# Kernel tuning notes

Measured on AMD Instinct MI355X. Metric: run time of the kernel, lower is better.

## Reference

```python
import jax, jax.numpy as jnp
import numpy as np

N = 100000   # total nodes in batch
E = 1200000  # total edges
D = 64       # dim_features (== hidden_dim)
H = 64       # hidden_dim
T = 32       # dim_targets
L = 3        # num_layers
G = 500      # number of graphs in batch


def setup_inputs() -> dict:
    key = jax.random.key(0)
    ks = jax.random.split(key, 16)
    s = 0.1
    inp = {
        "x": jax.random.normal(ks[0], (N, D), jnp.float32),
        "src": jax.random.randint(ks[1], (E,), 0, N, jnp.int32),
        "dst": jax.random.randint(ks[2], (E,), 0, N, jnp.int32),
        "graph_ids": jnp.sort(jax.random.randint(ks[3], (N,), 0, G, jnp.int32)),
        # GINConv learnable eps (init 0)
        "eps": jnp.zeros((L,), jnp.float32),
        # per-layer conv apply MLP: Linear(D->H), ReLU, Linear(H->H)
        "conv_w1": jax.random.normal(ks[4], (L, D, H), jnp.float32) * s,
        "conv_b1": jnp.zeros((L, H), jnp.float32),
        "conv_w2": jax.random.normal(ks[5], (L, H, H), jnp.float32) * s,
        "conv_b2": jnp.zeros((L, H), jnp.float32),
        # GraphNorm params
        "gn_weight": jnp.ones((L, H), jnp.float32),
        "gn_bias": jnp.zeros((L, H), jnp.float32),
        "gn_scale": jnp.ones((L, H), jnp.float32),
        # per-layer projection MLP: Linear(H->H), ReLU, Linear(H->T)
        "proj_w1": jax.random.normal(ks[6], (L, H, H), jnp.float32) * s,
        "proj_b1": jnp.zeros((L, H), jnp.float32),
        "proj_w2": jax.random.normal(ks[7], (L, H, T), jnp.float32) * s,
        "proj_b2": jnp.zeros((L, T), jnp.float32),
    }
    return inp


def reference(x, src, dst, graph_ids, eps, conv_w1, conv_b1, conv_w2, conv_b2,
              gn_weight, gn_bias, gn_scale, proj_w1, proj_b1, proj_w2, proj_b2):
    gid = graph_ids
    counts = jax.ops.segment_sum(jnp.ones((N,), x.dtype), gid, num_segments=G)
    safe = jnp.maximum(counts, 1.0)[:, None]  # [G,1] nodes per graph

    feat = x
    outs = []
    for l in range(L):
        # GINConv: (1+eps)*h_i + sum over incoming neighbors
        agg = jax.ops.segment_sum(feat[src], dst, num_segments=N)
        h = (1.0 + eps[l]) * feat + agg
        h = jnp.maximum(h @ conv_w1[l] + conv_b1[l], 0.0) @ conv_w2[l] + conv_b2[l]
        # GraphNorm: per-graph mean/std
        mean = jax.ops.segment_sum(h, gid, num_segments=G) / safe
        sub = h - mean[gid] * gn_scale[l]
        var = jax.ops.segment_sum(sub * sub, gid, num_segments=G) / safe
        std = jnp.sqrt(var + 1e-8)
        h = gn_weight[l] * sub / std[gid] + gn_bias[l]
        feat = jnp.maximum(h, 0.0)
        # projection MLP + per-graph mean pooling
        z = jnp.maximum(feat @ proj_w1[l] + proj_b1[l], 0.0) @ proj_w2[l] + proj_b2[l]
        outs.append(jax.ops.segment_sum(z, gid, num_segments=G) / safe)
    return jnp.concatenate(outs, axis=-1)  # [G, L*T]
```

## Files before the change

### kernel.cpp

```cpp
#include <hip/hip_runtime.h>
#include <math.h>

#define N_NODES 100000
#define N_EDGES 1200000
#define DIM 64
#define TDIM 32
#define NLAYERS 3
#define NGRAPH 500
#define NP (N_NODES + 1)

#define BUCKW 512
#define NBUCK ((N_NODES + BUCKW - 1) / BUCKW)
#define ECHUNK ((N_EDGES + 255) / 256)
#define MLPBL ((N_NODES + 63) / 64)

typedef unsigned short bfu;
typedef __attribute__((ext_vector_type(8))) short short8;
typedef __attribute__((ext_vector_type(4))) float v4f;

__device__ __forceinline__ float bf2f(bfu u) {
    union { unsigned int i; float f; } v; v.i = ((unsigned int)u) << 16; return v.f;
}
__device__ __forceinline__ float bflo(unsigned int d) {
    union { unsigned int i; float f; } v; v.i = d << 16; return v.f;
}
__device__ __forceinline__ float bfhi(unsigned int d) {
    union { unsigned int i; float f; } v; v.i = d & 0xFFFF0000u; return v.f;
}
__device__ __forceinline__ bfu f2bf(float f) {
    union { float f; unsigned int i; } v; v.f = f;
    unsigned int r = v.i + 0x7FFFu + ((v.i >> 16) & 1u);
    return (bfu)(r >> 16);
}

__global__ __launch_bounds__(256) void k_setup(const float* __restrict__ x, bfu* __restrict__ xb,
                                               const int* __restrict__ gid, int* __restrict__ gstart,
                                               float* __restrict__ inv_safe, float* __restrict__ ncnt,
                                               const float* __restrict__ w1, const float* __restrict__ w2,
                                               const float* __restrict__ q1, const float* __restrict__ q2,
                                               bfu* __restrict__ w1t, bfu* __restrict__ w2t,
                                               bfu* __restrict__ q1t, bfu* __restrict__ q2t,
                                               const int* __restrict__ dst, int* __restrict__ bcnt) {
    int b = blockIdx.x, t = threadIdx.x;
    if (b < 6250) {
        int base = (b * 256 + t) * 4;
        float4 v = *(const float4*)&x[base];
        ushort4 o;
        o.x = f2bf(v.x); o.y = f2bf(v.y); o.z = f2bf(v.z); o.w = f2bf(v.w);
        *(ushort4*)&xb[base] = o;
    } else if (b == 6250) {
        for (int tt = t; tt <= NGRAPH; tt += 256) {
            int lo = 0, hi = N_NODES;
            while (lo < hi) {
                int mid = (lo + hi) >> 1;
                if (gid[mid] < tt) lo = mid + 1; else hi = mid;
            }
            gstart[tt] = lo;
        }
        __syncthreads();
        for (int tt = t; tt < NGRAPH; tt += 256) {
            int c = gstart[tt + 1] - gstart[tt];
            inv_safe[tt] = 1.0f / (float)(c > 1 ? c : 1);
            ncnt[tt] = (float)c;
        }
    } else if (b < 6299) {
        int i = (b - 6251) * 256 + t;
        int l = i >> 12, k = (i >> 6) & 63, n = i & 63;
        int o = (l << 12) | (n << 6) | k;
        w1t[o] = f2bf(w1[i]);
        w2t[o] = f2bf(w2[i]);
        q1t[o] = f2bf(q1[i]);
        if (i < NLAYERS * 2048) {
            int l2 = i >> 11, rem = i & 2047, k2 = rem >> 5, n2 = rem & 31;
            q2t[l2 * 2048 + n2 * 64 + k2] = f2bf(q2[i]);
        }
    } else {
        __shared__ int h[NBUCK];
        for (int i = t; i < NBUCK; i += 256) h[i] = 0;
        __syncthreads();
        int e0 = (b - 6299) * ECHUNK;
        int e1 = e0 + ECHUNK; if (e1 > N_EDGES) e1 = N_EDGES;
        for (int e = e0 + t; e < e1; e += 256) atomicAdd(&h[dst[e] >> 9], 1);
        __syncthreads();
        for (int i = t; i < NBUCK; i += 256) if (h[i]) atomicAdd(&bcnt[i], h[i]);
    }
}

__global__ __launch_bounds__(256) void k_bscan(const int* __restrict__ bcnt,
                                               int* __restrict__ bbase, int* __restrict__ bcursor,
                                               const int* __restrict__ gstart,
                                               const float* __restrict__ pb2all, float* __restrict__ out) {
    __shared__ int s[256];
    int t = threadIdx.x;
    s[t] = (t < NBUCK) ? bcnt[t] : 0;
    __syncthreads();
    for (int off = 1; off < 256; off <<= 1) {
        int v = (t >= off) ? s[t - off] : 0;
        __syncthreads();
        s[t] += v;
        __syncthreads();
    }
    int ex = t ? s[t - 1] : 0;
    if (t < NBUCK) { bbase[t] = ex; bcursor[t] = ex; }
    if (t == 0) bbase[NBUCK] = N_EDGES;
    for (int g = t; g < NGRAPH; g += 256) {
        int nn = gstart[g + 1] - gstart[g];
        for (int r = 0; r < NLAYERS * TDIM; r++)
            out[g * (NLAYERS * TDIM) + r] = (nn > 0) ? pb2all[r] : 0.f;
    }
}

__global__ __launch_bounds__(256) void k_bscatter(const int* __restrict__ src, const int* __restrict__ dst,
                                                  int* __restrict__ bcursor, int2* __restrict__ ebuf) {
    __shared__ int cnt[NBUCK];
    __shared__ int base[NBUCK];
    int t = threadIdx.x;
    for (int i = t; i < NBUCK; i += 256) cnt[i] = 0;
    __syncthreads();
    int e0 = blockIdx.x * ECHUNK;
    int e1 = e0 + ECHUNK; if (e1 > N_EDGES) e1 = N_EDGES;
    for (int e = e0 + t; e < e1; e += 256) atomicAdd(&cnt[dst[e] >> 9], 1);
    __syncthreads();
    for (int i = t; i < NBUCK; i += 256) base[i] = cnt[i] ? atomicAdd(&bcursor[i], cnt[i]) : 0;
    __syncthreads();
    for (int i = t; i < NBUCK; i += 256) cnt[i] = 0;
    __syncthreads();
    for (int e = e0 + t; e < e1; e += 256) {
        int d = dst[e];
        int b = d >> 9;
        int r = atomicAdd(&cnt[b], 1);
        ebuf[base[b] + r] = make_int2(src[e], d);
    }
}

__global__ __launch_bounds__(256) void k_bcsr(const int2* __restrict__ ebuf, const int* __restrict__ bbase,
                                              int* __restrict__ offs, int* __restrict__ csr) {
    __shared__ int ldeg[BUCKW];
    __shared__ int lscan[BUCKW];
    __shared__ int lcur[BUCKW];
    int t = threadIdx.x;
    int b = blockIdx.x;
    int nbase = b << 9;
    int ebeg = bbase[b], eend = bbase[b + 1];
    ldeg[t] = 0; ldeg[t + 256] = 0;
    __syncthreads();
    for (int e = ebeg + t; e < eend; e += 256) atomicAdd(&ldeg[ebuf[e].y - nbase], 1);
    __syncthreads();
    lscan[t] = ldeg[t]; lscan[t + 256] = ldeg[t + 256];
    __syncthreads();
    for (int off = 1; off < BUCKW; off <<= 1) {
        int i0 = t, i1 = t + 256;
        int v0 = (i0 >= off) ? lscan[i0 - off] : 0;
        int v1 = (i1 >= off) ? lscan[i1 - off] : 0;
        __syncthreads();
        lscan[i0] += v0; lscan[i1] += v1;
        __syncthreads();
    }
    int ex0 = lscan[t] - ldeg[t];
    int ex1 = lscan[t + 256] - ldeg[t + 256];
    lcur[t] = ex0; lcur[t + 256] = ex1;
    int n0 = nbase + t, n1 = nbase + t + 256;
    if (n0 < N_NODES) offs[n0] = ebeg + ex0;
    if (n1 < N_NODES) offs[n1] = ebeg + ex1;
    if (b == 0 && t == 0) offs[N_NODES] = N_EDGES;
    __syncthreads();
    for (int e = ebeg + t; e < eend; e += 256) {
        int2 p = ebuf[e];
        int slot = atomicAdd(&lcur[p.y - nbase], 1);
        csr[ebeg + slot] = p.x;
    }
}

__global__ __launch_bounds__(256) void k_agg(const bfu* __restrict__ feat, const int* __restrict__ offs,
                                             const int* __restrict__ csr, const float* __restrict__ eps,
                                             int l, bfu* __restrict__ hin) {
    int t = threadIdx.x;
    int sub = t & 15;
    int node = blockIdx.x * 16 + (t >> 4);
    if (node >= N_NODES) return;
    int coff = sub * 4;
    int e0 = offs[node], e1 = offs[node + 1];
    int eL = e1 - 1;
    float acc0 = 0.f, acc1 = 0.f, acc2 = 0.f, acc3 = 0.f;

    for (int e = e0; e < e1; e += 2) {
        int eb = e + 1;
        int cb = (eb < e1) ? eb : eL;
        int sa = csr[e];
        int sb = csr[cb];
        uint2 da = *(const uint2*)&feat[sa * DIM + coff];
        uint2 db = *(const uint2*)&feat[sb * DIM + coff];
        if (eb >= e1) { db.x = 0u; db.y = 0u; }
        acc0 += bflo(da.x); acc1 += bfhi(da.x);
        acc2 += bflo(da.y); acc3 += bfhi(da.y);
        acc0 += bflo(db.x); acc1 += bfhi(db.x);
        acc2 += bflo(db.y); acc3 += bfhi(db.y);
    }

    float ep = 1.0f + eps[l];
    uint2 s = *(const uint2*)&feat[node * DIM + coff];
    float r0 = ep * bflo(s.x) + acc0;
    float r1 = ep * bfhi(s.x) + acc1;
    float r2 = ep * bflo(s.y) + acc2;
    float r3 = ep * bfhi(s.y) + acc3;
    uint2 o;
    o.x = ((unsigned int)f2bf(r1) << 16) | f2bf(r0);
    o.y = ((unsigned int)f2bf(r3) << 16) | f2bf(r2);
    *(uint2*)&hin[node * DIM + coff] = o;
}

__global__ __launch_bounds__(256) void k_mlp(const bfu* __restrict__ hin,
                                             const bfu* __restrict__ w1t, const float* __restrict__ b1,
                                             const bfu* __restrict__ w2t, const float* __restrict__ b2,
                                             const int* __restrict__ gid, bfu* __restrict__ hout,
                                             float* __restrict__ gsum, float* __restrict__ gsq) {
    __shared__ bfu ldsT[4][16 * 80];
    __shared__ int sG[4][16];
    int t = threadIdx.x;
    int w = t >> 6, lane = t & 63, m = lane & 15, q = lane >> 4;
    int nbase = blockIdx.x * 64 + w * 16;
    int row = nbase + m;
    bool valid = row < N_NODES;
    if (lane < 16) sG[w][lane] = (nbase + lane < N_NODES) ? gid[nbase + lane] : -1;

    short8 a0 = {0, 0, 0, 0, 0, 0, 0, 0}, a1 = a0;
    if (valid) {
        a0 = *(const short8*)&hin[row * 64 + q * 8];
        a1 = *(const short8*)&hin[row * 64 + 32 + q * 8];
    }
    short8 bf1[4][2], bf2[4][2];
#pragma unroll
    for (int ct = 0; ct < 4; ct++)
#pragma unroll
        for (int kk = 0; kk < 2; kk++) {
            bf1[ct][kk] = *(const short8*)&w1t[(ct * 16 + m) * 64 + kk * 32 + q * 8];
            bf2[ct][kk] = *(const short8*)&w2t[(ct * 16 + m) * 64 + kk * 32 + q * 8];
        }

    bfu* my = ldsT[w];
#pragma unroll
    for (int ct = 0; ct < 4; ct++) {
        float bv = b1[ct * 16 + m];
        v4f acc = {bv, bv, bv, bv};
        acc = __builtin_amdgcn_mfma_f32_16x16x32_bf16(a0, bf1[ct][0], acc, 0, 0, 0);
        acc = __builtin_amdgcn_mfma_f32_16x16x32_bf16(a1, bf1[ct][1], acc, 0, 0, 0);
#pragma unroll
        for (int r = 0; r < 4; r++)
            my[(q * 4 + r) * 80 + ct * 16 + m] = f2bf(fmaxf(acc[r], 0.f));
    }
    short8 a20 = *(short8*)&my[m * 80 + q * 8];
    short8 a21 = *(short8*)&my[m * 80 + 32 + q * 8];
#pragma unroll
    for (int ct = 0; ct < 4; ct++) {
        float bv = b2[ct * 16 + m];
        v4f acc = {bv, bv, bv, bv};
        acc = __builtin_amdgcn_mfma_f32_16x16x32_bf16(a20, bf2[ct][0], acc, 0, 0, 0);
        acc = __builtin_amdgcn_mfma_f32_16x16x32_bf16(a21, bf2[ct][1], acc, 0, 0, 0);
#pragma unroll
        for (int r = 0; r < 4; r++)
            my[(q * 4 + r) * 80 + ct * 16 + m] = f2bf(acc[r]);
    }
#pragma unroll
    for (int i = 0; i < 2; i++) {
        int idx = i * 64 + lane;
        int r = idx >> 3, ch = (idx & 7) * 8;
        int grow = nbase + r;
        uint4 v = *(uint4*)&my[r * 80 + ch];
        if (grow < N_NODES) *(uint4*)&hout[grow * 64 + ch] = v;
    }
    float s_acc = 0.f, q_acc = 0.f;
    int cur = sG[w][0];
    for (int r = 0; r < 16; r++) {
        int g2 = sG[w][r];
        if (g2 != cur) {
            if (cur >= 0) {
                atomicAdd(&gsum[cur * 64 + lane], s_acc);
                atomicAdd(&gsq[cur * 64 + lane], q_acc);
            }
            cur = g2; s_acc = 0.f; q_acc = 0.f;
        }
        if (g2 >= 0) {
            float v = bf2f(my[r * 80 + lane]);
            s_acc += v; q_acc += v * v;
        }
    }
    if (cur >= 0) {
        atomicAdd(&gsum[cur * 64 + lane], s_acc);
        atomicAdd(&gsq[cur * 64 + lane], q_acc);
    }
}

__global__ __launch_bounds__(256) void k_apply_proj(const bfu* __restrict__ h,
                                                    const int* __restrict__ gid,
                                                    const float* __restrict__ gsum,
                                                    const float* __restrict__ gsq,
                                                    const float* __restrict__ inv_safe,
                                                    const float* __restrict__ ncnt,
                                                    const float* __restrict__ gnw, const float* __restrict__ gnb,
                                                    const float* __restrict__ gns,
                                                    const bfu* __restrict__ p1t, const float* __restrict__ pb1,
                                                    const bfu* __restrict__ p2t,
                                                    bfu* __restrict__ feat, float* __restrict__ out, int l) {
    __shared__ bfu ldsT[4][16 * 80];
    __shared__ float sZ[64 * 33];
    __shared__ int sGid[64];
    int t = threadIdx.x;
    int w = t >> 6, lane = t & 63, m = lane & 15, q = lane >> 4;
    int row0 = blockIdx.x * 64;
    int row = row0 + w * 16 + m;
    bool valid = row < N_NODES;
    if (t < 64) sGid[t] = (row0 + t < N_NODES) ? gid[row0 + t] : -1;

    union Pack { short8 v; bfu u[8]; uint4 qv; };
    Pack a0, a1;
    a0.qv = make_uint4(0u, 0u, 0u, 0u);
    a1.qv = make_uint4(0u, 0u, 0u, 0u);
    if (valid) {
        int g = gid[row];
        float inv = inv_safe[g];
        float nnf = ncnt[g];
#pragma unroll
        for (int kk = 0; kk < 2; kk++) {
            int ch = kk * 32 + q * 8;
            uint4 hv = *(const uint4*)&h[row * 64 + ch];
            float4 Sa = *(const float4*)&gsum[g * 64 + ch];
            float4 Sb = *(const float4*)&gsum[g * 64 + ch + 4];
            float4 Qa = *(const float4*)&gsq[g * 64 + ch];
            float4 Qb = *(const float4*)&gsq[g * 64 + ch + 4];
            float4 nsa = *(const float4*)&gns[ch];
            float4 nsb = *(const float4*)&gns[ch + 4];
            float4 nwa = *(const float4*)&gnw[ch];
            float4 nwb = *(const float4*)&gnw[ch + 4];
            float4 gba = *(const float4*)&gnb[ch];
            float4 gbb = *(const float4*)&gnb[ch + 4];
            float hval[8] = {bflo(hv.x), bfhi(hv.x), bflo(hv.y), bfhi(hv.y),
                             bflo(hv.z), bfhi(hv.z), bflo(hv.w), bfhi(hv.w)};
            float Sv[8] = {Sa.x, Sa.y, Sa.z, Sa.w, Sb.x, Sb.y, Sb.z, Sb.w};
            float Qv[8] = {Qa.x, Qa.y, Qa.z, Qa.w, Qb.x, Qb.y, Qb.z, Qb.w};
            float nsv[8] = {nsa.x, nsa.y, nsa.z, nsa.w, nsb.x, nsb.y, nsb.z, nsb.w};
            float nwv[8] = {nwa.x, nwa.y, nwa.z, nwa.w, nwb.x, nwb.y, nwb.z, nwb.w};
            float gbv[8] = {gba.x, gba.y, gba.z, gba.w, gbb.x, gbb.y, gbb.z, gbb.w};
            Pack& a = kk ? a1 : a0;
#pragma unroll
            for (int j = 0; j < 8; j++) {
                float ms = Sv[j] * inv * nsv[j];
                float var = (Qv[j] - 2.f * ms * Sv[j] + nnf * ms * ms) * inv;
                float coef = nwv[j] * rsqrtf(var + 1e-8f);
                a.u[j] = f2bf(fmaxf(coef * (hval[j] - ms) + gbv[j], 0.f));
            }
            *(uint4*)&feat[row * 64 + ch] = a.qv;
        }
    }

    short8 bf1[4][2], bf2[2][2];
#pragma unroll
    for (int ct = 0; ct < 4; ct++)
#pragma unroll
        for (int kk = 0; kk < 2; kk++)
            bf1[ct][kk] = *(const short8*)&p1t[(ct * 16 + m) * 64 + kk * 32 + q * 8];
#pragma unroll
    for (int ct = 0; ct < 2; ct++)
#pragma unroll
        for (int kk = 0; kk < 2; kk++)
            bf2[ct][kk] = *(const short8*)&p2t[(ct * 16 + m) * 64 + kk * 32 + q * 8];

    bfu* tl = ldsT[w];
#pragma unroll
    for (int ct = 0; ct < 4; ct++) {
        float bv = pb1[ct * 16 + m];
        v4f acc = {bv, bv, bv, bv};
        acc = __builtin_amdgcn_mfma_f32_16x16x32_bf16(a0.v, bf1[ct][0], acc, 0, 0, 0);
        acc = __builtin_amdgcn_mfma_f32_16x16x32_bf16(a1.v, bf1[ct][1], acc, 0, 0, 0);
#pragma unroll
        for (int r = 0; r < 4; r++)
            tl[(q * 4 + r) * 80 + ct * 16 + m] = f2bf(fmaxf(acc[r], 0.f));
    }
    short8 a20 = *(short8*)&tl[m * 80 + q * 8];
    short8 a21 = *(short8*)&tl[m * 80 + 32 + q * 8];
#pragma unroll
    for (int ct = 0; ct < 2; ct++) {
        v4f acc = {0.f, 0.f, 0.f, 0.f};
        acc = __builtin_amdgcn_mfma_f32_16x16x32_bf16(a20, bf2[ct][0], acc, 0, 0, 0);
        acc = __builtin_amdgcn_mfma_f32_16x16x32_bf16(a21, bf2[ct][1], acc, 0, 0, 0);
#pragma unroll
        for (int r = 0; r < 4; r++)
            sZ[(w * 16 + q * 4 + r) * 33 + ct * 16 + m] = acc[r];
    }
    __syncthreads();

    if (t < 32) {
        int cur = sGid[0];
        float a = 0.f;
        for (int r = 0; r < 64; r++) {
            int g2 = sGid[r];
            if (g2 != cur) {
                if (cur >= 0) atomicAdd(&out[cur * (NLAYERS * TDIM) + l * TDIM + t], a * inv_safe[cur]);
                cur = g2;
                a = 0.f;
            }
            if (g2 >= 0) a += sZ[r * 33 + t];
        }
        if (cur >= 0) atomicAdd(&out[cur * (NLAYERS * TDIM) + l * TDIM + t], a * inv_safe[cur]);
    }
}


extern "C" void kernel_launch(void* const* d_in, const int* in_sizes, int n_in,
                              void* d_out, int out_size, void* d_ws, size_t ws_size,
                              hipStream_t stream) {
    const float* x        = (const float*)d_in[0];
    const int*   src      = (const int*)d_in[1];
    const int*   dst      = (const int*)d_in[2];
    const int*   gid      = (const int*)d_in[3];
    const float* eps      = (const float*)d_in[4];
    const float* conv_w1  = (const float*)d_in[5];
    const float* conv_b1  = (const float*)d_in[6];
    const float* conv_w2  = (const float*)d_in[7];
    const float* conv_b2  = (const float*)d_in[8];
    const float* gn_w     = (const float*)d_in[9];
    const float* gn_b     = (const float*)d_in[10];
    const float* gn_s     = (const float*)d_in[11];
    const float* proj_w1  = (const float*)d_in[12];
    const float* proj_b1  = (const float*)d_in[13];
    const float* proj_w2  = (const float*)d_in[14];
    const float* proj_b2  = (const float*)d_in[15];
    float* out = (float*)d_out;

    char* ws = (char*)d_ws;
    size_t off = 0;
    auto alloc = [&](size_t bytes) { char* p = ws + off; off += (bytes + 255) & ~(size_t)255; return p; };
    int*   offs     = (int*)alloc(NP * sizeof(int));
    int*   gstart   = (int*)alloc((NGRAPH + 1) * sizeof(int));
    float* inv_safe = (float*)alloc(NGRAPH * sizeof(float));
    float* ncnt     = (float*)alloc(NGRAPH * sizeof(float));
    int*   bcnt     = (int*)alloc(NBUCK * sizeof(int));
    float* gsumA    = (float*)alloc((size_t)NLAYERS * 2 * NGRAPH * 64 * sizeof(float));
    size_t zbytes   = (size_t)((char*)(gsumA + (size_t)NLAYERS * 2 * NGRAPH * 64) - (char*)bcnt);
    int*   bbase    = (int*)alloc((NBUCK + 1) * sizeof(int));
    int*   bcursor  = (int*)alloc(NBUCK * sizeof(int));
    int*   csr      = (int*)alloc(N_EDGES * sizeof(int));
    bfu*   featbf   = (bfu*)alloc((size_t)N_NODES * DIM * sizeof(bfu));
    bfu*   hinbf    = (bfu*)alloc((size_t)N_NODES * DIM * sizeof(bfu));
    bfu*   hbufbf   = (bfu*)alloc((size_t)N_NODES * DIM * sizeof(bfu));
    bfu*   w1t      = (bfu*)alloc((size_t)NLAYERS * 4096 * sizeof(bfu));
    bfu*   w2t      = (bfu*)alloc((size_t)NLAYERS * 4096 * sizeof(bfu));
    bfu*   p1t      = (bfu*)alloc((size_t)NLAYERS * 4096 * sizeof(bfu));
    bfu*   p2t      = (bfu*)alloc((size_t)NLAYERS * 2048 * sizeof(bfu));
    int2*  ebuf     = (int2*)alloc((size_t)N_EDGES * sizeof(int2));

    hipMemsetAsync(bcnt, 0, zbytes, stream);
    k_setup<<<6555, 256, 0, stream>>>(x, featbf, gid, gstart, inv_safe, ncnt,
                                      conv_w1, conv_w2, proj_w1, proj_w2, w1t, w2t, p1t, p2t,
                                      dst, bcnt);
    k_bscan<<<1, 256, 0, stream>>>(bcnt, bbase, bcursor, gstart, proj_b2, out);
    k_bscatter<<<256, 256, 0, stream>>>(src, dst, bcursor, ebuf);
    k_bcsr<<<NBUCK, 256, 0, stream>>>(ebuf, bbase, offs, csr);

    int aggbl = (N_NODES + 15) / 16;
    for (int l = 0; l < NLAYERS; l++) {
        float* gsum_l = gsumA + (size_t)l * 2 * NGRAPH * 64;
        float* gsq_l  = gsum_l + NGRAPH * 64;
        k_agg<<<aggbl, 256, 0, stream>>>(featbf, offs, csr, eps, l, hinbf);
        k_mlp<<<MLPBL, 256, 0, stream>>>(hinbf, w1t + l * 4096, conv_b1 + l * 64,
                                         w2t + l * 4096, conv_b2 + l * 64,
                                         gid, hbufbf, gsum_l, gsq_l);
        k_apply_proj<<<MLPBL, 256, 0, stream>>>(hbufbf, gid, gsum_l, gsq_l, inv_safe, ncnt,
                                                gn_w + l * 64, gn_b + l * 64, gn_s + l * 64,
                                                p1t + l * 4096, proj_b1 + l * 64,
                                                p2t + l * 2048, featbf, out, l);
    }
}
```

Measured before the change: 422.0 us.

## Fuse GIN neighbor aggregation into the conv MLP kernel via LDS staging

After: 428.1 us. Within noise of the previous version (+1.5%).

```diff
diff --git a/kernel.cpp b/kernel.cpp
--- a/kernel.cpp
+++ b/kernel.cpp
@@ -171,49 +171,13 @@
     }
 }
 
-__global__ __launch_bounds__(256) void k_agg(const bfu* __restrict__ feat, const int* __restrict__ offs,
-                                             const int* __restrict__ csr, const float* __restrict__ eps,
-                                             int l, bfu* __restrict__ hin) {
-    int t = threadIdx.x;
-    int sub = t & 15;
-    int node = blockIdx.x * 16 + (t >> 4);
-    if (node >= N_NODES) return;
-    int coff = sub * 4;
-    int e0 = offs[node], e1 = offs[node + 1];
-    int eL = e1 - 1;
-    float acc0 = 0.f, acc1 = 0.f, acc2 = 0.f, acc3 = 0.f;
-
-    for (int e = e0; e < e1; e += 2) {
-        int eb = e + 1;
-        int cb = (eb < e1) ? eb : eL;
-        int sa = csr[e];
-        int sb = csr[cb];
-        uint2 da = *(const uint2*)&feat[sa * DIM + coff];
-        uint2 db = *(const uint2*)&feat[sb * DIM + coff];
-        if (eb >= e1) { db.x = 0u; db.y = 0u; }
-        acc0 += bflo(da.x); acc1 += bfhi(da.x);
-        acc2 += bflo(da.y); acc3 += bfhi(da.y);
-        acc0 += bflo(db.x); acc1 += bfhi(db.x);
-        acc2 += bflo(db.y); acc3 += bfhi(db.y);
-    }
-
-    float ep = 1.0f + eps[l];
-    uint2 s = *(const uint2*)&feat[node * DIM + coff];
-    float r0 = ep * bflo(s.x) + acc0;
-    float r1 = ep * bfhi(s.x) + acc1;
-    float r2 = ep * bflo(s.y) + acc2;
-    float r3 = ep * bfhi(s.y) + acc3;
-    uint2 o;
-    o.x = ((unsigned int)f2bf(r1) << 16) | f2bf(r0);
-    o.y = ((unsigned int)f2bf(r3) << 16) | f2bf(r2);
-    *(uint2*)&hin[node * DIM + coff] = o;
-}
-
-__global__ __launch_bounds__(256) void k_mlp(const bfu* __restrict__ hin,
+__global__ __launch_bounds__(256) void k_mlp(const bfu* __restrict__ feat, const int* __restrict__ offs,
+                                             const int* __restrict__ csr, const float* __restrict__ eps, int l,
                                              const bfu* __restrict__ w1t, const float* __restrict__ b1,
                                              const bfu* __restrict__ w2t, const float* __restrict__ b2,
                                              const int* __restrict__ gid, bfu* __restrict__ hout,
                                              float* __restrict__ gsum, float* __restrict__ gsq) {
+    __shared__ bfu hstage[64 * 80];
     __shared__ bfu ldsT[4][16 * 80];
     __shared__ int sG[4][16];
     int t = threadIdx.x;
@@ -223,11 +187,52 @@
     bool valid = row < N_NODES;
     if (lane < 16) sG[w][lane] = (nbase + lane < N_NODES) ? gid[nbase + lane] : -1;
 
-    short8 a0 = {0, 0, 0, 0, 0, 0, 0, 0}, a1 = a0;
-    if (valid) {
-        a0 = *(const short8*)&hin[row * 64 + q * 8];
-        a1 = *(const short8*)&hin[row * 64 + 32 + q * 8];
-    }
+    {
+        int coff = (lane & 15) * 4;
+        int ng = lane >> 4;
+        float ep = 1.0f + eps[l];
+#pragma unroll
+        for (int s = 0; s < 4; s++) {
+            int nl = w * 16 + s * 4 + ng;
+            int node = blockIdx.x * 64 + nl;
+            float a0f = 0.f, a1f = 0.f, a2f = 0.f, a3f = 0.f;
+            if (node < N_NODES) {
+                int e0 = offs[node], e1 = offs[node + 1];
+                int eL = e1 - 1;
+                for (int e = e0; e < e1; e += 4) {
+                    int eb = e + 1, ec = e + 2, ed = e + 3;
+                    int cb = eb < e1 ? eb : eL;
+                    int cc = ec < e1 ? ec : eL;
+                    int cd = ed < e1 ? ed : eL;
+                    int sa = csr[e], sb = csr[cb], sc = csr[cc], sd = csr[cd];
+                    uint2 da = *(const uint2*)&feat[sa * DIM + coff];
+                    uint2 db = *(const uint2*)&feat[sb * DIM + coff];
+                    uint2 dc = *(const uint2*)&feat[sc * DIM + coff];
+                    uint2 dd = *(const uint2*)&feat[sd * DIM + coff];
+                    if (eb >= e1) { db.x = 0u; db.y = 0u; }
+                    if (ec >= e1) { dc.x = 0u; dc.y = 0u; }
+                    if (ed >= e1) { dd.x = 0u; dd.y = 0u; }
+                    a0f += bflo(da.x) + bflo(db.x) + bflo(dc.x) + bflo(dd.x);
+                    a1f += bfhi(da.x) + bfhi(db.x) + bfhi(dc.x) + bfhi(dd.x);
+                    a2f += bflo(da.y) + bflo(db.y) + bflo(dc.y) + bflo(dd.y);
+                    a3f += bfhi(da.y) + bfhi(db.y) + bfhi(dc.y) + bfhi(dd.y);
+                }
+                uint2 sv = *(const uint2*)&feat[node * DIM + coff];
+                a0f += ep * bflo(sv.x);
+                a1f += ep * bfhi(sv.x);
+                a2f += ep * bflo(sv.y);
+                a3f += ep * bfhi(sv.y);
+            }
+            uint2 o;
+            o.x = ((unsigned int)f2bf(a1f) << 16) | f2bf(a0f);
+            o.y = ((unsigned int)f2bf(a3f) << 16) | f2bf(a2f);
+            *(uint2*)&hstage[nl * 80 + coff] = o;
+        }
+    }
+
+    short8 a0 = *(const short8*)&hstage[(w * 16 + m) * 80 + q * 8];
+    short8 a1 = *(const short8*)&hstage[(w * 16 + m) * 80 + 32 + q * 8];
+
     short8 bf1[4][2], bf2[4][2];
 #pragma unroll
     for (int ct = 0; ct < 4; ct++)
@@ -440,7 +445,6 @@
     int*   bcursor  = (int*)alloc(NBUCK * sizeof(int));
     int*   csr      = (int*)alloc(N_EDGES * sizeof(int));
     bfu*   featbf   = (bfu*)alloc((size_t)N_NODES * DIM * sizeof(bfu));
-    bfu*   hinbf    = (bfu*)alloc((size_t)N_NODES * DIM * sizeof(bfu));
     bfu*   hbufbf   = (bfu*)alloc((size_t)N_NODES * DIM * sizeof(bfu));
     bfu*   w1t      = (bfu*)alloc((size_t)NLAYERS * 4096 * sizeof(bfu));
     bfu*   w2t      = (bfu*)alloc((size_t)NLAYERS * 4096 * sizeof(bfu));
@@ -456,12 +460,11 @@
     k_bscatter<<<256, 256, 0, stream>>>(src, dst, bcursor, ebuf);
     k_bcsr<<<NBUCK, 256, 0, stream>>>(ebuf, bbase, offs, csr);
 
-    int aggbl = (N_NODES + 15) / 16;
     for (int l = 0; l < NLAYERS; l++) {
         float* gsum_l = gsumA + (size_t)l * 2 * NGRAPH * 64;
         float* gsq_l  = gsum_l + NGRAPH * 64;
-        k_agg<<<aggbl, 256, 0, stream>>>(featbf, offs, csr, eps, l, hinbf);
-        k_mlp<<<MLPBL, 256, 0, stream>>>(hinbf, w1t + l * 4096, conv_b1 + l * 64,
+        k_mlp<<<MLPBL, 256, 0, stream>>>(featbf, offs, csr, eps, l,
+                                         w1t + l * 4096, conv_b1 + l * 64,
                                          w2t + l * 4096, conv_b2 + l * 64,
                                          gid, hbufbf, gsum_l, gsq_l);
         k_apply_proj<<<MLPBL, 256, 0, stream>>>(hbufbf, gid, gsum_l, gsq_l, inv_safe, ncnt,
```
